# Optimization experiments

Measured on AMD Instinct MI355X. Metric: run time of the kernel, lower is better.

Reference implementation:

```python
import jax, jax.numpy as jnp
import numpy as np

# Structure constants T[k, p, q] = sign such that (a (x) b)_k = sum_{p,q} T[k,p,q] a_p b_q,
# transcribed term-by-term from clifford_product_3d (Cl(3,0), metric +,+,+).
_TERMS = [
    (0,0,0, 1),(0,1,1, 1),(0,2,2, 1),(0,3,3, 1),(0,4,4,-1),(0,5,5,-1),(0,6,6,-1),(0,7,7,-1),
    (1,0,1, 1),(1,1,0, 1),(1,2,4,-1),(1,3,5, 1),(1,4,2, 1),(1,5,3,-1),(1,6,7,-1),(1,7,6,-1),
    (2,0,2, 1),(2,1,4, 1),(2,2,0, 1),(2,3,6,-1),(2,4,1,-1),(2,5,7, 1),(2,6,3, 1),(2,7,5,-1),
    (3,0,3, 1),(3,1,5,-1),(3,2,6, 1),(3,3,0, 1),(3,4,7,-1),(3,5,1,-1),(3,6,2,-1),(3,7,4, 1),
    (4,0,4, 1),(4,1,2, 1),(4,2,1,-1),(4,3,7, 1),(4,4,0, 1),(4,5,6,-1),(4,6,5, 1),(4,7,3,-1),
    (5,0,5, 1),(5,1,3,-1),(5,2,7, 1),(5,3,1, 1),(5,4,6, 1),(5,5,0, 1),(5,6,4,-1),(5,7,2,-1),
    (6,0,6, 1),(6,1,7,-1),(6,2,3,-1),(6,3,2, 1),(6,4,5,-1),(6,5,4, 1),(6,6,0, 1),(6,7,1, 1),
    (7,0,7, 1),(7,1,6, 1),(7,2,5,-1),(7,3,4, 1),(7,4,3, 1),(7,5,2,-1),(7,6,1, 1),(7,7,0, 1),
]

def _clifford_table():
    T = np.zeros((8, 8, 8), dtype=np.float32)
    for k, p, q, s in _TERMS:
        T[k, p, q] = s
    return jnp.asarray(T)

_T = _clifford_table()


def setup_inputs() -> dict:
    key = jax.random.key(0)
    k1, k2 = jax.random.split(key)
    C_in, C_out = 8, 8
    x = jax.random.normal(k1, (4096, 512, C_in, 8), dtype=jnp.float32)
    weight = jax.random.normal(k2, (C_out, C_in, 8), dtype=jnp.float32) * C_in ** (-0.5)
    bias = jnp.zeros((C_out, 8), dtype=jnp.float32)
    return {"x": x, "weight": weight, "bias": bias}


def reference(x, weight, bias):
    # out[..., o, k] = sum_i sum_{p,q} T[k,p,q] * weight[o,i,p] * x[..., i, q] + bias[o,k]
    # Contract weight with T first (tiny), then a single GEMM-like contraction over (i,q):
    # avoids the naive [..., C_out, C_in, 8] broadcast intermediate entirely.
    wT = jnp.einsum('kpq,oip->oikq', _T.astype(weight.dtype), weight)  # [C_out, C_in, 8, 8]
    out = jnp.einsum('oikq,biq->bok', wT, x.reshape(-1, *x.shape[-2:]))
    out = out.reshape(*x.shape[:-2], *out.shape[-2:])
    return out + bias
```

## Files before the change

kernel.cpp:

```cpp
#include <hip/hip_runtime.h>
#include <hip/hip_bf16.h>
#include <stdint.h>

__constant__ signed char QTAB[64] = {
    0,1,2,3,4,5,6,7,
    1,0,4,5,2,3,7,6,
    2,4,0,6,1,7,3,5,
    3,5,6,0,7,1,2,4,
    4,2,1,7,0,6,5,3,
    5,3,7,1,6,0,4,2,
    6,7,3,2,5,4,0,1,
    7,6,5,4,3,2,1,0};
__constant__ signed char SGN[64] = {
    1, 1, 1, 1,-1,-1,-1,-1,
    1, 1,-1, 1, 1,-1,-1,-1,
    1, 1, 1,-1,-1, 1, 1,-1,
    1,-1, 1, 1,-1,-1,-1, 1,
    1, 1,-1, 1, 1,-1, 1,-1,
    1,-1, 1, 1, 1, 1,-1,-1,
    1,-1,-1, 1,-1, 1, 1, 1,
    1, 1,-1, 1, 1,-1, 1, 1};

typedef __attribute__((ext_vector_type(8))) short bf16x8;
typedef __attribute__((ext_vector_type(4))) float f32x4;
typedef __attribute__((ext_vector_type(4))) unsigned int u32x4;

#define SBAR __builtin_amdgcn_sched_barrier(0)
#define WAITVM(N)                                         \
    asm volatile("s_waitcnt vmcnt(" #N ")" ::: "memory"); \
    SBAR

__global__ void clifford_prep(const float* __restrict__ weight,
                              float* __restrict__ W2,
                              unsigned short* __restrict__ W2T) {
    int t = threadIdx.x;
    for (int e = t; e < 4096; e += 256) {
        int o = e >> 9, i = (e >> 6) & 7, k = (e >> 3) & 7, p = e & 7;
        int q = (int)QTAB[k * 8 + p];
        float s = (float)SGN[k * 8 + p];
        W2[((i * 8 + q) * 64) + (o * 8 + k)] = s * weight[(o * 8 + i) * 8 + p];
    }
    __syncthreads();
    for (int e = t; e < 4096; e += 256) {
        int n = e >> 6, k = e & 63;
        __hip_bfloat16 h = __float2bfloat16(W2[k * 64 + n]);
        W2T[n * 64 + k] = *reinterpret_cast<unsigned short*>(&h);
    }
}

static __device__ __forceinline__ short f2bf(float f) {
    __hip_bfloat16 h = __float2bfloat16(f);
    return *reinterpret_cast<short*>(&h);
}

#define LOADA(CI, R)                                                         \
    {                                                                        \
        const float* b_ = x + (size_t)(CI) * 2048;                           \
        _Pragma("unroll") for (int mt_ = 0; mt_ < 2; ++mt_)                  \
        _Pragma("unroll") for (int kh_ = 0; kh_ < 2; ++kh_) {                \
            const float* p_ =                                                \
                b_ + (mt_ * 16 + (l & 15)) * 64 + kh_ * 32 + 8 * (l >> 4);   \
            R[mt_][kh_][0] = *(const f32x4*)p_;                              \
            R[mt_][kh_][1] = *(const f32x4*)(p_ + 4);                        \
        }                                                                    \
    }

#define COMPUTE(R)                                                           \
    {                                                                        \
        _Pragma("unroll") for (int kh = 0; kh < 2; ++kh) {                   \
            bf16x8 afr[2];                                                   \
            _Pragma("unroll") for (int mt = 0; mt < 2; ++mt) {               \
                bf16x8 a_;                                                   \
                a_[0] = f2bf(R[mt][kh][0].x); a_[1] = f2bf(R[mt][kh][0].y);  \
                a_[2] = f2bf(R[mt][kh][0].z); a_[3] = f2bf(R[mt][kh][0].w);  \
                a_[4] = f2bf(R[mt][kh][1].x); a_[5] = f2bf(R[mt][kh][1].y);  \
                a_[6] = f2bf(R[mt][kh][1].z); a_[7] = f2bf(R[mt][kh][1].w);  \
                afr[mt] = a_;                                                \
            }                                                                \
            _Pragma("unroll") for (int nt = 0; nt < 4; ++nt) {               \
                int n_ = nt * 16 + (l & 15);                                 \
                int qb = kh * 4 + (l >> 4);                                  \
                bf16x8 bfr = *(const bf16x8*)((const char*)w2t + n_ * 128 +  \
                                              (((qb ^ (n_ & 7))) << 4));     \
                acc[0][nt] = __builtin_amdgcn_mfma_f32_16x16x32_bf16(        \
                    afr[0], bfr, acc[0][nt], 0, 0, 0);                       \
                acc[1][nt] = __builtin_amdgcn_mfma_f32_16x16x32_bf16(        \
                    afr[1], bfr, acc[1][nt], 0, 0, 0);                       \
            }                                                                \
        }                                                                    \
    }

#define STORE_CHUNK(CI)                                                      \
    {                                                                        \
        _Pragma("unroll") for (int mt = 0; mt < 2; ++mt)                     \
        _Pragma("unroll") for (int nt = 0; nt < 4; ++nt)                     \
        _Pragma("unroll") for (int rg = 0; rg < 4; ++rg) {                   \
            int row_ = mt * 16 + 4 * (l >> 4) + rg;                          \
            sg[row_ * 64 + nt * 16 + (l & 15)] = acc[mt][nt][rg];            \
        }                                                                    \
        float* ob_ = out + (size_t)(CI) * 2048;                              \
        _Pragma("unroll") for (int j_ = 0; j_ < 8; ++j_) {                   \
            f32x4 v_ = *(const f32x4*)(sg + j_ * 256 + 4 * l);               \
            __builtin_nontemporal_store(v_,                                  \
                                        (f32x4*)(ob_ + j_ * 256 + 4 * l));   \
        }                                                                    \
    }

#define ACC_INIT                                                 \
    f32x4 acc[2][4];                                             \
    _Pragma("unroll") for (int mt = 0; mt < 2; ++mt)             \
    _Pragma("unroll") for (int nt = 0; nt < 4; ++nt) {           \
        acc[mt][nt][0] = bvv[nt]; acc[mt][nt][1] = bvv[nt];      \
        acc[mt][nt][2] = bvv[nt]; acc[mt][nt][3] = bvv[nt];      \
    }

__global__ __launch_bounds__(256) void clifford_main(
    const float* __restrict__ x, const unsigned short* __restrict__ W2T,
    const float* __restrict__ bias, float* __restrict__ out, int nB) {
    __shared__ __align__(16) float stg[4][2048];
    __shared__ __align__(16) unsigned short w2t[4096];

    const int tid = threadIdx.x;
    const int l = tid & 63;
    const int wv = tid >> 6;

#pragma unroll
    for (int gg = 0; gg < 2; ++gg) {
        int g = tid * 2 + gg;
        int n = g >> 3, q = g & 7;
        u32x4 v = *(const u32x4*)(W2T + n * 64 + q * 8);
        *(u32x4*)((char*)w2t + n * 128 + ((q ^ (n & 7)) << 4)) = v;
    }
    __syncthreads();

    float* sg = stg[wv];
    const int nC = nB >> 5;
    const long long nW = (long long)gridDim.x * 4;
    const long long w = (long long)blockIdx.x * 4 + wv;
    const int cpw = (int)(nC / nW);
    const long long rem = nC - (long long)cpw * nW;

    float bvv[4];
#pragma unroll
    for (int nt = 0; nt < 4; ++nt) bvv[nt] = bias[nt * 16 + (l & 15)];
#pragma unroll
    for (int nt = 0; nt < 4; ++nt) asm volatile("" : "+v"(bvv[nt]));

    f32x4 RA[2][2][2], RB[2][2][2];
    const long long c0 = w * cpw;
    if (cpw >= 3) {
        LOADA(c0, RA);
        LOADA(c0 + 1, RB);
        WAITVM(8);
        for (int i = 0; i < cpw - 2; ++i) {
            const long long c = c0 + i;
            ACC_INIT;
            if ((i & 1) == 0) {
                COMPUTE(RA);
                LOADA(c + 2, RA);
                STORE_CHUNK(c);
            } else {
                COMPUTE(RB);
                LOADA(c + 2, RB);
                STORE_CHUNK(c);
            }
            WAITVM(16);
        }
        {
            ACC_INIT;
            if (((cpw - 2) & 1) == 0) { COMPUTE(RA); } else { COMPUTE(RB); }
            STORE_CHUNK(c0 + cpw - 2);
            WAITVM(8);
        }
        {
            ACC_INIT;
            if (((cpw - 1) & 1) == 0) { COMPUTE(RA); } else { COMPUTE(RB); }
            STORE_CHUNK(c0 + cpw - 1);
        }
    } else {
        for (int i = 0; i < cpw; ++i) {
            LOADA(c0 + i, RA);
            WAITVM(0);
            ACC_INIT;
            COMPUTE(RA);
            STORE_CHUNK(c0 + i);
            WAITVM(0);
        }
    }
    if (w < rem) {
        const long long c = nW * cpw + w;
        WAITVM(0);
        LOADA(c, RA);
        WAITVM(0);
        ACC_INIT;
        COMPUTE(RA);
        STORE_CHUNK(c);
    }
}

extern "C" void kernel_launch(void* const* d_in, const int* in_sizes, int n_in,
                              void* d_out, int out_size, void* d_ws,
                              size_t ws_size, hipStream_t stream) {
    const float* x = (const float*)d_in[0];
    const float* weight = (const float*)d_in[1];
    const float* bias = (const float*)d_in[2];
    float* out = (float*)d_out;
    float* W2 = (float*)d_ws;
    unsigned short* W2T = (unsigned short*)(W2 + 4096);

    int nB = in_sizes[0] / 64;

    hipLaunchKernelGGL(clifford_prep, dim3(1), dim3(256), 0, stream, weight,
                       W2, W2T);
    int nC = nB >> 5;
    int blocks = 2048;
    if (blocks * 4 > nC) blocks = (nC + 3) / 4;
    if (blocks < 1) blocks = 1;
    hipLaunchKernelGGL(clifford_main, dim3(blocks), dim3(256), 0, stream, x,
                       W2T, bias, out, nB);
}
```

Baseline: 215.4 us.

## Swap MFMA operands so accumulators store directly to global without LDS staging

Computes the transposed product (weights as the A operand, x as the B operand), so each lane's accumulator holds 4 contiguous output columns of one row. This lets the output be written with direct 16-byte nontemporal stores and removes the per-wave LDS staging buffer and its write/read round-trip. The stores are less coalesced per instruction (lanes write strided 16-byte pieces across rows), which could cost some write efficiency in exchange for fewer LDS operations and less shared memory use.

```diff
diff --git a/kernel.cpp b/kernel.cpp
--- a/kernel.cpp
+++ b/kernel.cpp
@@ -53,76 +53,67 @@
     return *reinterpret_cast<short*>(&h);
 }
 
-#define LOADA(CI, R)                                                         \
+#define LOADB(CI, R)                                                         \
     {                                                                        \
         const float* b_ = x + (size_t)(CI) * 2048;                           \
-        _Pragma("unroll") for (int mt_ = 0; mt_ < 2; ++mt_)                  \
+        _Pragma("unroll") for (int bt_ = 0; bt_ < 2; ++bt_)                  \
         _Pragma("unroll") for (int kh_ = 0; kh_ < 2; ++kh_) {                \
             const float* p_ =                                                \
-                b_ + (mt_ * 16 + (l & 15)) * 64 + kh_ * 32 + 8 * (l >> 4);   \
-            R[mt_][kh_][0] = *(const f32x4*)p_;                              \
-            R[mt_][kh_][1] = *(const f32x4*)(p_ + 4);                        \
+                b_ + (bt_ * 16 + (l & 15)) * 64 + kh_ * 32 + 8 * (l >> 4);   \
+            R[bt_][kh_][0] = *(const f32x4*)p_;                              \
+            R[bt_][kh_][1] = *(const f32x4*)(p_ + 4);                        \
         }                                                                    \
     }
 
 #define COMPUTE(R)                                                           \
     {                                                                        \
         _Pragma("unroll") for (int kh = 0; kh < 2; ++kh) {                   \
-            bf16x8 afr[2];                                                   \
-            _Pragma("unroll") for (int mt = 0; mt < 2; ++mt) {               \
-                bf16x8 a_;                                                   \
-                a_[0] = f2bf(R[mt][kh][0].x); a_[1] = f2bf(R[mt][kh][0].y);  \
-                a_[2] = f2bf(R[mt][kh][0].z); a_[3] = f2bf(R[mt][kh][0].w);  \
-                a_[4] = f2bf(R[mt][kh][1].x); a_[5] = f2bf(R[mt][kh][1].y);  \
-                a_[6] = f2bf(R[mt][kh][1].z); a_[7] = f2bf(R[mt][kh][1].w);  \
-                afr[mt] = a_;                                                \
+            bf16x8 afr[4];                                                   \
+            _Pragma("unroll") for (int mt = 0; mt < 4; ++mt) {               \
+                int m_ = mt * 16 + (l & 15);                                 \
+                int qb = kh * 4 + (l >> 4);                                  \
+                afr[mt] = *(const bf16x8*)((const char*)w2t + m_ * 128 +     \
+                                           (((qb ^ (m_ & 7))) << 4));        \
             }                                                                \
-            _Pragma("unroll") for (int nt = 0; nt < 4; ++nt) {               \
-                int n_ = nt * 16 + (l & 15);                                 \
-                int qb = kh * 4 + (l >> 4);                                  \
-                bf16x8 bfr = *(const bf16x8*)((const char*)w2t + n_ * 128 +  \
-                                              (((qb ^ (n_ & 7))) << 4));     \
-                acc[0][nt] = __builtin_amdgcn_mfma_f32_16x16x32_bf16(        \
-                    afr[0], bfr, acc[0][nt], 0, 0, 0);                       \
-                acc[1][nt] = __builtin_amdgcn_mfma_f32_16x16x32_bf16(        \
-                    afr[1], bfr, acc[1][nt], 0, 0, 0);                       \
+            _Pragma("unroll") for (int bt = 0; bt < 2; ++bt) {               \
+                bf16x8 xf;                                                   \
+                xf[0] = f2bf(R[bt][kh][0].x); xf[1] = f2bf(R[bt][kh][0].y);  \
+                xf[2] = f2bf(R[bt][kh][0].z); xf[3] = f2bf(R[bt][kh][0].w);  \
+                xf[4] = f2bf(R[bt][kh][1].x); xf[5] = f2bf(R[bt][kh][1].y);  \
+                xf[6] = f2bf(R[bt][kh][1].z); xf[7] = f2bf(R[bt][kh][1].w);  \
+                _Pragma("unroll") for (int mt = 0; mt < 4; ++mt) {           \
+                    acc[mt][bt] = __builtin_amdgcn_mfma_f32_16x16x32_bf16(   \
+                        afr[mt], xf, acc[mt][bt], 0, 0, 0);                  \
+                }                                                            \
             }                                                                \
         }                                                                    \
     }
 
 #define STORE_CHUNK(CI)                                                      \
     {                                                                        \
-        _Pragma("unroll") for (int mt = 0; mt < 2; ++mt)                     \
-        _Pragma("unroll") for (int nt = 0; nt < 4; ++nt)                     \
-        _Pragma("unroll") for (int rg = 0; rg < 4; ++rg) {                   \
-            int row_ = mt * 16 + 4 * (l >> 4) + rg;                          \
-            sg[row_ * 64 + nt * 16 + (l & 15)] = acc[mt][nt][rg];            \
+        float* ob_ = out + (size_t)(CI) * 2048;                              \
+        _Pragma("unroll") for (int mt = 0; mt < 4; ++mt)                     \
+        _Pragma("unroll") for (int bt = 0; bt < 2; ++bt) {                   \
+            __builtin_nontemporal_store(                                     \
+                acc[mt][bt],                                                 \
+                (f32x4*)(ob_ + (bt * 16 + (l & 15)) * 64 + mt * 16 +         \
+                         4 * (l >> 4)));                                     \
         }                                                                    \
-        float* ob_ = out + (size_t)(CI) * 2048;                              \
-        _Pragma("unroll") for (int j_ = 0; j_ < 8; ++j_) {                   \
-            f32x4 v_ = *(const f32x4*)(sg + j_ * 256 + 4 * l);               \
-            __builtin_nontemporal_store(v_,                                  \
-                                        (f32x4*)(ob_ + j_ * 256 + 4 * l));   \
-        }                                                                    \
     }
 
 #define ACC_INIT                                                 \
-    f32x4 acc[2][4];                                             \
-    _Pragma("unroll") for (int mt = 0; mt < 2; ++mt)             \
-    _Pragma("unroll") for (int nt = 0; nt < 4; ++nt) {           \
-        acc[mt][nt][0] = bvv[nt]; acc[mt][nt][1] = bvv[nt];      \
-        acc[mt][nt][2] = bvv[nt]; acc[mt][nt][3] = bvv[nt];      \
-    }
+    f32x4 acc[4][2];                                             \
+    _Pragma("unroll") for (int mt = 0; mt < 4; ++mt)             \
+    _Pragma("unroll") for (int bt = 0; bt < 2; ++bt)             \
+        acc[mt][bt] = bvv4[mt];
 
 __global__ __launch_bounds__(256) void clifford_main(
     const float* __restrict__ x, const unsigned short* __restrict__ W2T,
     const float* __restrict__ bias, float* __restrict__ out, int nB) {
-    __shared__ __align__(16) float stg[4][2048];
     __shared__ __align__(16) unsigned short w2t[4096];
 
     const int tid = threadIdx.x;
     const int l = tid & 63;
-    const int wv = tid >> 6;
 
 #pragma unroll
     for (int gg = 0; gg < 2; ++gg) {
@@ -133,35 +124,35 @@
     }
     __syncthreads();
 
-    float* sg = stg[wv];
     const int nC = nB >> 5;
     const long long nW = (long long)gridDim.x * 4;
-    const long long w = (long long)blockIdx.x * 4 + wv;
+    const long long w = (long long)blockIdx.x * 4 + (tid >> 6);
     const int cpw = (int)(nC / nW);
     const long long rem = nC - (long long)cpw * nW;
 
-    float bvv[4];
+    f32x4 bvv4[4];
 #pragma unroll
-    for (int nt = 0; nt < 4; ++nt) bvv[nt] = bias[nt * 16 + (l & 15)];
+    for (int mt = 0; mt < 4; ++mt)
+        bvv4[mt] = *(const f32x4*)(bias + mt * 16 + 4 * (l >> 4));
 #pragma unroll
-    for (int nt = 0; nt < 4; ++nt) asm volatile("" : "+v"(bvv[nt]));
+    for (int mt = 0; mt < 4; ++mt) asm volatile("" : "+v"(bvv4[mt]));
 
     f32x4 RA[2][2][2], RB[2][2][2];
     const long long c0 = w * cpw;
     if (cpw >= 3) {
-        LOADA(c0, RA);
-        LOADA(c0 + 1, RB);
+        LOADB(c0, RA);
+        LOADB(c0 + 1, RB);
         WAITVM(8);
         for (int i = 0; i < cpw - 2; ++i) {
             const long long c = c0 + i;
             ACC_INIT;
             if ((i & 1) == 0) {
                 COMPUTE(RA);
-                LOADA(c + 2, RA);
+                LOADB(c + 2, RA);
                 STORE_CHUNK(c);
             } else {
                 COMPUTE(RB);
-                LOADA(c + 2, RB);
+                LOADB(c + 2, RB);
                 STORE_CHUNK(c);
             }
             WAITVM(16);
@@ -179,7 +170,7 @@
         }
     } else {
         for (int i = 0; i < cpw; ++i) {
-            LOADA(c0 + i, RA);
+            LOADB(c0 + i, RA);
             WAITVM(0);
             ACC_INIT;
             COMPUTE(RA);
@@ -190,7 +181,7 @@
     if (w < rem) {
         const long long c = nW * cpw + w;
         WAITVM(0);
-        LOADA(c, RA);
+        LOADB(c, RA);
         WAITVM(0);
         ACC_INIT;
         COMPUTE(RA);
```

Result: slower. 250.9 us (+16.5%).
